# Kernel tuning notes

Measured on AMD Instinct MI355X. Metric: run time of the kernel, lower is better.

The kernel has to match this reference:

```python
import jax, jax.numpy as jnp
import numpy as np

N_NODES = 50000
N_EDGES = 800000
DIM_A = 96
DIM_V = 64
R0 = 2.0
LEAK = 0.1
EPS = 1e-12


def radial_encode_8(r_vec, r0):
    # Soft one-hot (tent) radial basis over 8 bins on [0, r0].
    r = jnp.linalg.norm(r_vec, axis=-1)                      # [E]
    u = r * (8.0 / r0)
    k = jnp.arange(8, dtype=r.dtype)
    return jax.nn.relu(1.0 - jnp.abs(u[..., None] - k))      # [E, 8]


def tens_sigmoid_rank1(x):
    # Equivariant norm-squashing of a rank-1 tensor: direction kept, norm -> tanh(norm).
    n = jnp.linalg.norm(x, axis=-1, keepdims=True)
    return x * (jnp.tanh(n) / jnp.maximum(n, EPS))


def leaky(x):
    return jnp.where(x >= 0, x, LEAK * x)


def setup_inputs() -> dict:
    key = jax.random.key(0)
    ks = jax.random.split(key, 8)
    s = lambda k, sh, fan: jax.random.normal(k, sh, jnp.float32) / np.float32(np.sqrt(fan))
    r_ij = jax.random.normal(ks[0], (N_EDGES, 3), jnp.float32)
    src = jax.random.randint(ks[1], (N_EDGES,), 0, N_NODES, jnp.int32)
    return {
        "r_ij": r_ij,
        "w0": s(ks[2], (DIM_A, 8), 8),   "b0": jnp.zeros((DIM_A,), jnp.float32),
        "w1": s(ks[3], (DIM_A, DIM_A), DIM_A), "b1": jnp.zeros((DIM_A,), jnp.float32),
        "w2": s(ks[4], (DIM_A, DIM_A), DIM_A), "b2": jnp.zeros((DIM_A,), jnp.float32),
        "w3": s(ks[5], (DIM_A, DIM_A), DIM_A),
        "wv": s(ks[6], (DIM_V, DIM_A), DIM_A),
        "src": src,
    }


def reference(r_ij, w0, b0, w1, b1, w2, b2, w3, wv, src):
    # Per-edge radial MLP: Linear(8,da) -> [Linear, LeakyReLU, Linear, LeakyReLU, Linear(no bias)]
    enc = radial_encode_8(r_ij, R0)                          # [E, 8]
    h = enc @ w0.T + b0                                      # [E, da]
    h = leaky(h @ w1.T + b1)
    h = leaky(h @ w2.T + b2)
    rad = h @ w3.T                                           # [E, da]
    rv = tens_sigmoid_rank1(r_ij * (7.0 / R0))               # [E, 3]
    phi_v = rad[:, :, None] * rv[:, None, :]                 # [E, da, 3]
    A_a = jax.ops.segment_sum(rad, src, num_segments=N_NODES)     # [N, da]
    A_v = jax.ops.segment_sum(phi_v, src, num_segments=N_NODES)   # [N, da, 3]
    out_v = jnp.einsum('va,nac->nvc', wv, A_v)               # [N, dv, 3]
    return (A_a, out_v)
```

## Files before the change

kernel.cpp:

```cpp
#include <hip/hip_runtime.h>
#include <math.h>

typedef float f32x4 __attribute__((ext_vector_type(4)));
typedef short s16x8 __attribute__((ext_vector_type(8)));

__device__ __forceinline__ unsigned short f2bf(float f) {
    unsigned u = __builtin_bit_cast(unsigned, f);
    u += 0x7fffu + ((u >> 16) & 1u);
    return (unsigned short)(u >> 16);
}

#define PACK_TOT 36864

__global__ __launch_bounds__(256) void pack_weights_k(
    const float* __restrict__ w0, const float* __restrict__ w1,
    const float* __restrict__ w2, const float* __restrict__ w3,
    const float* __restrict__ wv, unsigned short* __restrict__ dst)
{
    int idx = blockIdx.x * 256 + threadIdx.x;
    if (idx >= PACK_TOT) return;
    const float* W; int inF, ntiles, off;
    if (idx < 3072)       { W = w0; inF = 8;  ntiles = 6; off = 0; }
    else if (idx < 12288) { W = w1; inF = 96; ntiles = 6; off = 3072; }
    else if (idx < 21504) { W = w2; inF = 96; ntiles = 6; off = 12288; }
    else if (idx < 30720) { W = w3; inF = 96; ntiles = 6; off = 21504; }
    else                  { W = wv; inF = 96; ntiles = 4; off = 30720; }
    int r  = idx - off;
    int fi = r >> 9;
    int wi = r & 511;
    int l = wi >> 3, j = wi & 7;
    int kt = fi / ntiles, nt = fi - kt * ntiles;
    int n = nt * 16 + (l & 15);
    int k = kt * 32 + ((l >> 4) << 3) + j;
    float v = (k < inF) ? W[n * inF + k] : 0.0f;
    dst[idx] = f2bf(v);
}

__global__ __launch_bounds__(256) void hist_k(const int* __restrict__ src,
                                              int* __restrict__ counts, int E)
{
    int e = blockIdx.x * 256 + threadIdx.x;
    if (e < E) atomicAdd(&counts[src[e]], 1);
}

__global__ __launch_bounds__(256) void scan1_k(const int* __restrict__ counts,
                                               int* __restrict__ cursor,
                                               int* __restrict__ bsum, int N)
{
    __shared__ int wsum_s[4];
    int b = blockIdx.x, t = threadIdx.x, lane = t & 63, wid = t >> 6;
    int i0 = b * 2048 + t * 8;
    int v[8]; int s = 0;
    #pragma unroll
    for (int j = 0; j < 8; j++) { int i = i0 + j; v[j] = (i < N) ? counts[i] : 0; s += v[j]; }
    int inc = s;
    #pragma unroll
    for (int d = 1; d < 64; d <<= 1) { int o = __shfl_up(inc, d, 64); if (lane >= d) inc += o; }
    if (lane == 63) wsum_s[wid] = inc;
    __syncthreads();
    int wb = 0;
    for (int k = 0; k < wid; k++) wb += wsum_s[k];
    int run = wb + inc - s;
    #pragma unroll
    for (int j = 0; j < 8; j++) { int i = i0 + j; if (i < N) cursor[i] = run; run += v[j]; }
    if (t == 255) bsum[b] = wb + inc;
}

__global__ __launch_bounds__(64) void scan2_k(int* __restrict__ bsum, int nb)
{
    int lane = threadIdx.x;
    int v = (lane < nb) ? bsum[lane] : 0;
    int inc = v;
    #pragma unroll
    for (int d = 1; d < 64; d <<= 1) { int o = __shfl_up(inc, d, 64); if (lane >= d) inc += o; }
    if (lane < nb) bsum[lane] = inc - v;
}

__global__ __launch_bounds__(256) void scatter_k(const int* __restrict__ src,
                                                 const float* __restrict__ r_ij,
                                                 const int* __restrict__ bsum,
                                                 int* __restrict__ cursor,
                                                 int* __restrict__ order,
                                                 int* __restrict__ srcs,
                                                 float4* __restrict__ rsrt,
                                                 int use_rsrt, int E)
{
    int e = blockIdx.x * 256 + threadIdx.x;
    if (e < E) {
        int s = src[e];
        int p = bsum[s >> 11] + atomicAdd(&cursor[s], 1);
        if (use_rsrt) {
            rsrt[p] = make_float4(r_ij[3*e], r_ij[3*e+1], r_ij[3*e+2], __int_as_float(s));
        } else {
            order[p] = e;
            srcs[p] = s;
        }
    }
}

__global__ __launch_bounds__(256, 3) void edge_kernel(
    const float* __restrict__ r_ij,
    const int* __restrict__ order, const int* __restrict__ srcs,
    const float4* __restrict__ rsrt, int use_rsrt,
    const unsigned short* __restrict__ wp,
    const float* __restrict__ b0, const float* __restrict__ b1, const float* __restrict__ b2,
    float* __restrict__ A_a, float* __restrict__ Ov, int E)
{
    __shared__ unsigned short h_s[128 * 104];
    __shared__ unsigned short vfrag_s[16 * 512];
    __shared__ unsigned short rvb_s[3 * 128];
    __shared__ unsigned char  segid_s[128];
    __shared__ int  segnode_s[128];
    __shared__ int  src_s[128];
    __shared__ int  nseg_s;

    const int tid = threadIdx.x;
    const int w  = tid >> 6;
    const int l  = tid & 63;
    const int e0 = blockIdx.x * 128;
    const int lr = l & 15;
    const int lg = l >> 4;
    const int mbase = w * 32;

    if (l < 32) {
        const int ml = mbase + l;
        const int pos = e0 + ml;
        float x = 0.f, y = 0.f, z = 0.f; int s = -1;
        if (pos < E) {
            if (use_rsrt) {
                float4 v4 = rsrt[pos];
                x = v4.x; y = v4.y; z = v4.z; s = __float_as_int(v4.w);
            } else {
                int e = order[pos];
                s = srcs[pos];
                x = r_ij[3*e]; y = r_ij[3*e+1]; z = r_ij[3*e+2];
            }
        }
        float r = sqrtf(x*x + y*y + z*z);
        float u = r * 4.0f;
        s16x8 ev;
        #pragma unroll
        for (int k = 0; k < 8; k++) {
            float t = fmaxf(1.0f - fabsf(u - (float)k), 0.0f);
            ev[k] = (short)f2bf((s >= 0) ? t : 0.0f);
        }
        *(s16x8*)&h_s[ml * 104 + 96] = ev;
        float nn = 3.5f * r;
        float sc = (s >= 0) ? (3.5f * tanhf(nn) / fmaxf(nn, 1e-12f)) : 0.0f;
        rvb_s[0*128 + ml] = f2bf(x * sc);
        rvb_s[1*128 + ml] = f2bf(y * sc);
        rvb_s[2*128 + ml] = f2bf(z * sc);
        src_s[ml] = s;
    }
    __syncthreads();

    if (w == 0) {
        int i = l;
        int sA = src_s[i];
        bool fA = (i == 0) || (sA != src_s[i - 1]);
        unsigned long long mA = __ballot(fA);
        unsigned long long maskA = (~0ull) >> (63 - i);
        int incA = (int)__popcll(mA & maskA);
        segid_s[i] = (unsigned char)(incA - 1);
        if (fA) segnode_s[incA - 1] = sA;
        int totA = (int)__popcll(mA);
        int jrow = 64 + i;
        int sB = src_s[jrow];
        bool fB = (sB != src_s[jrow - 1]);
        unsigned long long mB = __ballot(fB);
        int incB = (int)__popcll(mB & maskA);
        segid_s[jrow] = (unsigned char)(totA + incB - 1);
        if (fB) segnode_s[totA + incB - 1] = sB;
        if (i == 63) nseg_s = totA + (int)__popcll(mB);
    }

    float b0v[6], b1v[6], b2v[6];
    #pragma unroll
    for (int nt = 0; nt < 6; nt++) {
        b0v[nt] = b0[nt*16 + lr];
        b1v[nt] = b1[nt*16 + lr];
        b2v[nt] = b2[nt*16 + lr];
    }

    {
        s16x8 A0[2];
        #pragma unroll
        for (int mf = 0; mf < 2; mf++) {
            s16x8 a = {0,0,0,0,0,0,0,0};
            if (l < 16) a = *(const s16x8*)&h_s[(mbase + mf*16 + lr) * 104 + 96];
            A0[mf] = a;
        }
        f32x4 acc[2][6];
        #pragma unroll
        for (int nt = 0; nt < 6; nt++) {
            s16x8 B = *(const s16x8*)&wp[nt * 512 + l * 8];
            f32x4 z4 = {0.f,0.f,0.f,0.f};
            acc[0][nt] = __builtin_amdgcn_mfma_f32_16x16x32_bf16(A0[0], B, z4, 0, 0, 0);
            acc[1][nt] = __builtin_amdgcn_mfma_f32_16x16x32_bf16(A0[1], B, z4, 0, 0, 0);
        }
        #pragma unroll
        for (int mf = 0; mf < 2; mf++)
        #pragma unroll
        for (int nt = 0; nt < 6; nt++)
        #pragma unroll
        for (int j = 0; j < 4; j++)
            h_s[(mbase + mf*16 + lg*4 + j) * 104 + nt*16 + lr] = f2bf(acc[mf][nt][j] + b0v[nt]);
    }

    #pragma unroll
    for (int li = 0; li < 2; li++) {
        const int poff = 3072 + li * 9216;
        s16x8 A[2][3];
        #pragma unroll
        for (int mf = 0; mf < 2; mf++)
        #pragma unroll
        for (int kt = 0; kt < 3; kt++)
            A[mf][kt] = *(const s16x8*)&h_s[(mbase + mf*16 + lr) * 104 + kt*32 + lg*8];
        f32x4 a2[2][6] = {};
        #pragma unroll
        for (int nt = 0; nt < 6; nt++)
        #pragma unroll
        for (int kt = 0; kt < 3; kt++) {
            s16x8 B = *(const s16x8*)&wp[poff + (kt*6 + nt) * 512 + l * 8];
            a2[0][nt] = __builtin_amdgcn_mfma_f32_16x16x32_bf16(A[0][kt], B, a2[0][nt], 0, 0, 0);
            a2[1][nt] = __builtin_amdgcn_mfma_f32_16x16x32_bf16(A[1][kt], B, a2[1][nt], 0, 0, 0);
        }
        #pragma unroll
        for (int mf = 0; mf < 2; mf++)
        #pragma unroll
        for (int nt = 0; nt < 6; nt++)
        #pragma unroll
        for (int j = 0; j < 4; j++) {
            float v = a2[mf][nt][j] + ((li == 0) ? b1v[nt] : b2v[nt]);
            v = (v >= 0.f) ? v : 0.1f * v;
            h_s[(mbase + mf*16 + lg*4 + j) * 104 + nt*16 + lr] = f2bf(v);
        }
    }

    uint2 radp[2][6];
    {
        s16x8 A[2][3];
        #pragma unroll
        for (int mf = 0; mf < 2; mf++)
        #pragma unroll
        for (int kt = 0; kt < 3; kt++)
            A[mf][kt] = *(const s16x8*)&h_s[(mbase + mf*16 + lr) * 104 + kt*32 + lg*8];
        f32x4 rad[2][6] = {};
        #pragma unroll
        for (int nt = 0; nt < 6; nt++)
        #pragma unroll
        for (int kt = 0; kt < 3; kt++) {
            s16x8 B = *(const s16x8*)&wp[21504 + (kt*6 + nt) * 512 + l * 8];
            rad[0][nt] = __builtin_amdgcn_mfma_f32_16x16x32_bf16(A[0][kt], B, rad[0][nt], 0, 0, 0);
            rad[1][nt] = __builtin_amdgcn_mfma_f32_16x16x32_bf16(A[1][kt], B, rad[1][nt], 0, 0, 0);
        }
        #pragma unroll
        for (int mf = 0; mf < 2; mf++)
        #pragma unroll
        for (int nt = 0; nt < 6; nt++) {
            unsigned short q0 = f2bf(rad[mf][nt][0]);
            unsigned short q1 = f2bf(rad[mf][nt][1]);
            unsigned short q2 = f2bf(rad[mf][nt][2]);
            unsigned short q3 = f2bf(rad[mf][nt][3]);
            radp[mf][nt].x = (unsigned)q0 | ((unsigned)q1 << 16);
            radp[mf][nt].y = (unsigned)q2 | ((unsigned)q3 << 16);
            h_s[(mbase + mf*16 + lg*4 + 0) * 104 + nt*16 + lr] = q0;
            h_s[(mbase + mf*16 + lg*4 + 1) * 104 + nt*16 + lr] = q1;
            h_s[(mbase + mf*16 + lg*4 + 2) * 104 + nt*16 + lr] = q2;
            h_s[(mbase + mf*16 + lg*4 + 3) * 104 + nt*16 + lr] = q3;
        }
    }

    f32x4 av[2][4] = {};
    {
        s16x8 Ar[2][3];
        #pragma unroll
        for (int mf = 0; mf < 2; mf++)
        #pragma unroll
        for (int kt = 0; kt < 3; kt++)
            Ar[mf][kt] = *(const s16x8*)&h_s[(mbase + mf*16 + lr) * 104 + kt*32 + lg*8];
        #pragma unroll
        for (int vt = 0; vt < 4; vt++)
        #pragma unroll
        for (int kt = 0; kt < 3; kt++) {
            s16x8 B = *(const s16x8*)&wp[30720 + (kt*4 + vt) * 512 + l * 8];
            av[0][vt] = __builtin_amdgcn_mfma_f32_16x16x32_bf16(Ar[0][kt], B, av[0][vt], 0, 0, 0);
            av[1][vt] = __builtin_amdgcn_mfma_f32_16x16x32_bf16(Ar[1][kt], B, av[1][vt], 0, 0, 0);
        }
    }

    __syncthreads();

    #pragma unroll
    for (int mf = 0; mf < 2; mf++)
    #pragma unroll
    for (int nt = 0; nt < 6; nt++)
        *(uint2*)&h_s[(w*6 + nt) * 512 + ((2*mf + (lg>>1))*16 + lr) * 8 + (lg&1)*4] = radp[mf][nt];

    #pragma unroll
    for (int mf = 0; mf < 2; mf++)
    #pragma unroll
    for (int vt = 0; vt < 4; vt++) {
        unsigned short q0 = f2bf(av[mf][vt][0]);
        unsigned short q1 = f2bf(av[mf][vt][1]);
        unsigned short q2 = f2bf(av[mf][vt][2]);
        unsigned short q3 = f2bf(av[mf][vt][3]);
        uint2 p; p.x = (unsigned)q0 | ((unsigned)q1 << 16); p.y = (unsigned)q2 | ((unsigned)q3 << 16);
        *(uint2*)&vfrag_s[(w*4 + vt) * 512 + ((2*mf + (lg>>1))*16 + lr) * 8 + (lg&1)*4] = p;
    }

    __syncthreads();

    const int nseg = nseg_s;
    if (w == 0) {
        for (int st = 0; st * 16 < nseg; ++st) {
            const int target = st * 16 + lr;
            f32x4 acc[6] = {};
            #pragma unroll
            for (int kt = 0; kt < 4; kt++) {
                uint2 sid8 = *(const uint2*)&segid_s[kt*32 + 8*lg];
                s16x8 af;
                #pragma unroll
                for (int j = 0; j < 8; j++) {
                    unsigned word = (j < 4) ? sid8.x : sid8.y;
                    int sid = (word >> (8 * (j & 3))) & 255;
                    af[j] = (short)((sid == target) ? 0x3F80 : 0);
                }
                #pragma unroll
                for (int nt = 0; nt < 6; nt++) {
                    s16x8 B = *(const s16x8*)&h_s[(kt*6 + nt) * 512 + l * 8];
                    acc[nt] = __builtin_amdgcn_mfma_f32_16x16x32_bf16(af, B, acc[nt], 0, 0, 0);
                }
            }
            #pragma unroll
            for (int nt = 0; nt < 6; nt++)
            #pragma unroll
            for (int j = 0; j < 4; j++) {
                int g = st*16 + 4*lg + j;
                if (g < nseg) {
                    int node = segnode_s[g];
                    if (node >= 0)
                        unsafeAtomicAdd(&A_a[node*96 + nt*16 + lr], acc[nt][j]);
                }
            }
        }
    } else {
        const int c = w - 1;
        for (int st = 0; st * 16 < nseg; ++st) {
            const int target = st * 16 + lr;
            f32x4 acc[4] = {};
            #pragma unroll
            for (int kt = 0; kt < 4; kt++) {
                uint2 sid8 = *(const uint2*)&segid_s[kt*32 + 8*lg];
                s16x8 rv8 = *(const s16x8*)&rvb_s[c*128 + kt*32 + 8*lg];
                s16x8 af;
                #pragma unroll
                for (int j = 0; j < 8; j++) {
                    unsigned word = (j < 4) ? sid8.x : sid8.y;
                    int sid = (word >> (8 * (j & 3))) & 255;
                    af[j] = (sid == target) ? rv8[j] : (short)0;
                }
                #pragma unroll
                for (int vt = 0; vt < 4; vt++) {
                    s16x8 B = *(const s16x8*)&vfrag_s[(kt*4 + vt) * 512 + l * 8];
                    acc[vt] = __builtin_amdgcn_mfma_f32_16x16x32_bf16(af, B, acc[vt], 0, 0, 0);
                }
            }
            #pragma unroll
            for (int vt = 0; vt < 4; vt++)
            #pragma unroll
            for (int j = 0; j < 4; j++) {
                int g = st*16 + 4*lg + j;
                if (g < nseg) {
                    int node = segnode_s[g];
                    if (node >= 0)
                        unsafeAtomicAdd(&Ov[node*192 + (vt*16 + lr)*3 + c], acc[vt][j]);
                }
            }
        }
    }
}

extern "C" void kernel_launch(void* const* d_in, const int* in_sizes, int n_in,
                              void* d_out, int out_size, void* d_ws, size_t ws_size,
                              hipStream_t stream)
{
    const float* r_ij = (const float*)d_in[0];
    const float* w0   = (const float*)d_in[1];
    const float* b0   = (const float*)d_in[2];
    const float* w1   = (const float*)d_in[3];
    const float* b1   = (const float*)d_in[4];
    const float* w2   = (const float*)d_in[5];
    const float* b2   = (const float*)d_in[6];
    const float* w3   = (const float*)d_in[7];
    const float* wv   = (const float*)d_in[8];
    const int*   src  = (const int*)d_in[9];
    const int E = in_sizes[0] / 3;
    const int N = out_size / 288;
    float* A_a = (float*)d_out;
    float* Ov  = A_a + (size_t)N * 96;

    char* wsb = (char*)d_ws;
    unsigned short* wp = (unsigned short*)wsb;
    size_t off = 73728;
    int* counts = (int*)(wsb + off);  off += (((size_t)N*4 + 127) & ~127ull);
    int* cursor = (int*)(wsb + off);  off += (((size_t)N*4 + 127) & ~127ull);
    int* bsum   = (int*)(wsb + off);  off += 256;
    size_t need_rsrt = off + (size_t)E * 16;
    int use_rsrt = (need_rsrt <= ws_size) ? 1 : 0;
    float4* rsrt = (float4*)(wsb + off);
    int* order   = (int*)(wsb + off);
    int* srcs    = (int*)(wsb + off + (((size_t)E*4 + 127) & ~127ull));

    const int nb = (N + 2047) / 2048;

    hipMemsetAsync(d_out, 0, (size_t)out_size * sizeof(float), stream);
    hipMemsetAsync(counts, 0, (size_t)N * 4, stream);

    pack_weights_k<<<(PACK_TOT + 255) / 256, 256, 0, stream>>>(w0, w1, w2, w3, wv, wp);
    hist_k<<<(E + 255) / 256, 256, 0, stream>>>(src, counts, E);
    scan1_k<<<nb, 256, 0, stream>>>(counts, cursor, bsum, N);
    scan2_k<<<1, 64, 0, stream>>>(bsum, nb);
    scatter_k<<<(E + 255) / 256, 256, 0, stream>>>(src, r_ij, bsum, cursor,
                                                   order, srcs, rsrt, use_rsrt, E);
    edge_kernel<<<(E + 127) / 128, 256, 0, stream>>>(r_ij, order, srcs, rsrt, use_rsrt,
                                                     wp, b0, b1, b2, A_a, Ov, E);
}
```

Before: 270.1 us.

## Apply wv after segment reduction and fold biases into MFMA accumulators

The per-edge wv projection (128x96 by 96x64 per block) is removed. The wv matrix is now applied after the per-segment reduction in the three vector-channel waves: rad is first reduced per segment weighted by rv, then staged to LDS and multiplied by wv. This cuts per-edge MFMA work and drops the vfrag_s LDS buffer, which frees shared memory so the launch bound can rise to 4 blocks per SU. Biases are also loaded as the initial MFMA accumulators, and leaky ReLU becomes fmaxf. The cost is extra work per segment tile: an LDS round trip and 12 extra MFMAs per segment tile for each of the three waves. The output also takes an extra bf16 rounding of the segment sums.

Measured after the change: 274.4 us. About the same (+1.6%).

```diff
diff --git a/kernel.cpp b/kernel.cpp
--- a/kernel.cpp
+++ b/kernel.cpp
@@ -98,7 +98,7 @@
     }
 }
 
-__global__ __launch_bounds__(256, 3) void edge_kernel(
+__global__ __launch_bounds__(256, 4) void edge_kernel(
     const float* __restrict__ r_ij,
     const int* __restrict__ order, const int* __restrict__ srcs,
     const float4* __restrict__ rsrt, int use_rsrt,
@@ -106,8 +106,7 @@
     const float* __restrict__ b0, const float* __restrict__ b1, const float* __restrict__ b2,
     float* __restrict__ A_a, float* __restrict__ Ov, int E)
 {
-    __shared__ unsigned short h_s[128 * 104];
-    __shared__ unsigned short vfrag_s[16 * 512];
+    __shared__ unsigned short h_s[16896];
     __shared__ unsigned short rvb_s[3 * 128];
     __shared__ unsigned char  segid_s[128];
     __shared__ int  segnode_s[128];
@@ -194,9 +193,9 @@
         #pragma unroll
         for (int nt = 0; nt < 6; nt++) {
             s16x8 B = *(const s16x8*)&wp[nt * 512 + l * 8];
-            f32x4 z4 = {0.f,0.f,0.f,0.f};
-            acc[0][nt] = __builtin_amdgcn_mfma_f32_16x16x32_bf16(A0[0], B, z4, 0, 0, 0);
-            acc[1][nt] = __builtin_amdgcn_mfma_f32_16x16x32_bf16(A0[1], B, z4, 0, 0, 0);
+            f32x4 bi = {b0v[nt], b0v[nt], b0v[nt], b0v[nt]};
+            acc[0][nt] = __builtin_amdgcn_mfma_f32_16x16x32_bf16(A0[0], B, bi, 0, 0, 0);
+            acc[1][nt] = __builtin_amdgcn_mfma_f32_16x16x32_bf16(A0[1], B, bi, 0, 0, 0);
         }
         #pragma unroll
         for (int mf = 0; mf < 2; mf++)
@@ -204,7 +203,7 @@
         for (int nt = 0; nt < 6; nt++)
         #pragma unroll
         for (int j = 0; j < 4; j++)
-            h_s[(mbase + mf*16 + lg*4 + j) * 104 + nt*16 + lr] = f2bf(acc[mf][nt][j] + b0v[nt]);
+            h_s[(mbase + mf*16 + lg*4 + j) * 104 + nt*16 + lr] = f2bf(acc[mf][nt][j]);
     }
 
     #pragma unroll
@@ -216,7 +215,13 @@
         #pragma unroll
         for (int kt = 0; kt < 3; kt++)
             A[mf][kt] = *(const s16x8*)&h_s[(mbase + mf*16 + lr) * 104 + kt*32 + lg*8];
-        f32x4 a2[2][6] = {};
+        f32x4 a2[2][6];
+        #pragma unroll
+        for (int nt = 0; nt < 6; nt++) {
+            float bb = (li == 0) ? b1v[nt] : b2v[nt];
+            f32x4 bi = {bb, bb, bb, bb};
+            a2[0][nt] = bi; a2[1][nt] = bi;
+        }
         #pragma unroll
         for (int nt = 0; nt < 6; nt++)
         #pragma unroll
@@ -231,8 +236,8 @@
         for (int nt = 0; nt < 6; nt++)
         #pragma unroll
         for (int j = 0; j < 4; j++) {
-            float v = a2[mf][nt][j] + ((li == 0) ? b1v[nt] : b2v[nt]);
-            v = (v >= 0.f) ? v : 0.1f * v;
+            float v = a2[mf][nt][j];
+            v = fmaxf(v, 0.1f * v);
             h_s[(mbase + mf*16 + lg*4 + j) * 104 + nt*16 + lr] = f2bf(v);
         }
     }
@@ -264,28 +269,6 @@
             unsigned short q3 = f2bf(rad[mf][nt][3]);
             radp[mf][nt].x = (unsigned)q0 | ((unsigned)q1 << 16);
             radp[mf][nt].y = (unsigned)q2 | ((unsigned)q3 << 16);
-            h_s[(mbase + mf*16 + lg*4 + 0) * 104 + nt*16 + lr] = q0;
-            h_s[(mbase + mf*16 + lg*4 + 1) * 104 + nt*16 + lr] = q1;
-            h_s[(mbase + mf*16 + lg*4 + 2) * 104 + nt*16 + lr] = q2;
-            h_s[(mbase + mf*16 + lg*4 + 3) * 104 + nt*16 + lr] = q3;
-        }
-    }
-
-    f32x4 av[2][4] = {};
-    {
-        s16x8 Ar[2][3];
-        #pragma unroll
-        for (int mf = 0; mf < 2; mf++)
-        #pragma unroll
-        for (int kt = 0; kt < 3; kt++)
-            Ar[mf][kt] = *(const s16x8*)&h_s[(mbase + mf*16 + lr) * 104 + kt*32 + lg*8];
-        #pragma unroll
-        for (int vt = 0; vt < 4; vt++)
-        #pragma unroll
-        for (int kt = 0; kt < 3; kt++) {
-            s16x8 B = *(const s16x8*)&wp[30720 + (kt*4 + vt) * 512 + l * 8];
-            av[0][vt] = __builtin_amdgcn_mfma_f32_16x16x32_bf16(Ar[0][kt], B, av[0][vt], 0, 0, 0);
-            av[1][vt] = __builtin_amdgcn_mfma_f32_16x16x32_bf16(Ar[1][kt], B, av[1][vt], 0, 0, 0);
         }
     }
 
@@ -296,18 +279,6 @@
     #pragma unroll
     for (int nt = 0; nt < 6; nt++)
         *(uint2*)&h_s[(w*6 + nt) * 512 + ((2*mf + (lg>>1))*16 + lr) * 8 + (lg&1)*4] = radp[mf][nt];
-
-    #pragma unroll
-    for (int mf = 0; mf < 2; mf++)
-    #pragma unroll
-    for (int vt = 0; vt < 4; vt++) {
-        unsigned short q0 = f2bf(av[mf][vt][0]);
-        unsigned short q1 = f2bf(av[mf][vt][1]);
-        unsigned short q2 = f2bf(av[mf][vt][2]);
-        unsigned short q3 = f2bf(av[mf][vt][3]);
-        uint2 p; p.x = (unsigned)q0 | ((unsigned)q1 << 16); p.y = (unsigned)q2 | ((unsigned)q3 << 16);
-        *(uint2*)&vfrag_s[(w*4 + vt) * 512 + ((2*mf + (lg>>1))*16 + lr) * 8 + (lg&1)*4] = p;
-    }
 
     __syncthreads();
 
@@ -346,9 +317,10 @@
         }
     } else {
         const int c = w - 1;
+        const int scb = 12288 + (w - 1) * 1536;
         for (int st = 0; st * 16 < nseg; ++st) {
             const int target = st * 16 + lr;
-            f32x4 acc[4] = {};
+            f32x4 acc6[6] = {};
             #pragma unroll
             for (int kt = 0; kt < 4; kt++) {
                 uint2 sid8 = *(const uint2*)&segid_s[kt*32 + 8*lg];
@@ -361,10 +333,32 @@
                     af[j] = (sid == target) ? rv8[j] : (short)0;
                 }
                 #pragma unroll
-                for (int vt = 0; vt < 4; vt++) {
-                    s16x8 B = *(const s16x8*)&vfrag_s[(kt*4 + vt) * 512 + l * 8];
-                    acc[vt] = __builtin_amdgcn_mfma_f32_16x16x32_bf16(af, B, acc[vt], 0, 0, 0);
-                }
+                for (int nt = 0; nt < 6; nt++) {
+                    s16x8 B = *(const s16x8*)&h_s[(kt*6 + nt) * 512 + l * 8];
+                    acc6[nt] = __builtin_amdgcn_mfma_f32_16x16x32_bf16(af, B, acc6[nt], 0, 0, 0);
+                }
+            }
+            #pragma unroll
+            for (int nt = 0; nt < 6; nt++) {
+                int ktf = nt >> 1;
+                int lane2 = ((nt & 1) * 2 + (lr >> 3)) * 16 + 4*lg;
+                int a0 = scb + ktf*512 + lane2*8 + (lr & 7);
+                h_s[a0]      = f2bf(acc6[nt][0]);
+                h_s[a0 + 8]  = f2bf(acc6[nt][1]);
+                h_s[a0 + 16] = f2bf(acc6[nt][2]);
+                h_s[a0 + 24] = f2bf(acc6[nt][3]);
+            }
+            s16x8 As[3];
+            #pragma unroll
+            for (int ktf = 0; ktf < 3; ktf++)
+                As[ktf] = *(const s16x8*)&h_s[scb + ktf*512 + l*8];
+            f32x4 acc2[4] = {};
+            #pragma unroll
+            for (int vt = 0; vt < 4; vt++)
+            #pragma unroll
+            for (int ktf = 0; ktf < 3; ktf++) {
+                s16x8 B = *(const s16x8*)&wp[30720 + (ktf*4 + vt) * 512 + l * 8];
+                acc2[vt] = __builtin_amdgcn_mfma_f32_16x16x32_bf16(As[ktf], B, acc2[vt], 0, 0, 0);
             }
             #pragma unroll
             for (int vt = 0; vt < 4; vt++)
@@ -374,7 +368,7 @@
                 if (g < nseg) {
                     int node = segnode_s[g];
                     if (node >= 0)
-                        unsafeAtomicAdd(&Ov[node*192 + (vt*16 + lr)*3 + c], acc[vt][j]);
+                        unsafeAtomicAdd(&Ov[node*192 + (vt*16 + lr)*3 + c], acc2[vt][j]);
                 }
             }
         }
```
